# Kernel tuning notes

Hardware: AMD Instinct MI355X
Metric: run time of the kernel (lower is better)

## Reference

```python
import jax, jax.numpy as jnp
import numpy as np

B, T = 1024, 320
EEG_CH, GEO_CH, F1, HID, OUT = 64, 18, 8, 32, 4
THETA0, BETA, TAU_A = 0.5, 1.8, 0.36
EPS = 1e-5


def _bn(x, s, b, m, v):
    # eval-mode BatchNorm with running stats (flax default eps 1e-5)
    return (x - m) * jax.lax.rsqrt(v + EPS) * s + b


def _dwconv(x, w, b, groups):
    # depthwise temporal conv, x: (B, T, C), w: (K, 1, C*F1), SAME padding
    y = jax.lax.conv_general_dilated(x, w, (1,), 'SAME', dimension_numbers=('NWC', 'WIO', 'NWC'), feature_group_count=groups)
    return y + b


def _spike(x):
    return jnp.where(x >= 0.0, 1.0, 0.0)


def _forward(x_eeg, x_geo, eeg_conv_w, eeg_conv_b, eeg_bn1_s, eeg_bn1_b, eeg_bn1_m, eeg_bn1_v, eeg_dense_w, eeg_dense_b, eeg_bn2_s, eeg_bn2_b, eeg_bn2_m, eeg_bn2_v, geo_conv_w, geo_conv_b, geo_bn1_s, geo_bn1_b, geo_bn1_m, geo_bn1_v, geo_dense_w, geo_dense_b, geo_bn2_s, geo_bn2_b, geo_bn2_m, geo_bn2_v, gamma, fc1_w, fc1_b, fc2_w, fc2_b):
    Bc = x_eeg.shape[0]
    xe = _bn(_dwconv(x_eeg, eeg_conv_w, eeg_conv_b, EEG_CH), eeg_bn1_s, eeg_bn1_b, eeg_bn1_m, eeg_bn1_v)
    xe = _bn(xe @ eeg_dense_w + eeg_dense_b, eeg_bn2_s, eeg_bn2_b, eeg_bn2_m, eeg_bn2_v)
    eeg_enc = jax.nn.relu(xe)                      # (B, T, HID)
    xg = _bn(_dwconv(x_geo, geo_conv_w, geo_conv_b, GEO_CH), geo_bn1_s, geo_bn1_b, geo_bn1_m, geo_bn1_v)
    xg = _bn(xg @ geo_dense_w + geo_dense_b, geo_bn2_s, geo_bn2_b, geo_bn2_m, geo_bn2_v)
    geo_mod = jax.nn.sigmoid(xg)                   # (B, T, HID)

    def step(carry, inp):
        m1, m2, m3, ma, eta, mli, prev = carry
        ce, cg = inp
        m1 = 0.9 * m1 + ce; s1 = _spike(m1 - 0.7); m1 = m1 * (1.0 - s1)
        m2 = 0.8 * m2 + ce; s2 = _spike(m2 - 0.5); m2 = m2 * (1.0 - s2)
        m3 = 0.6 * m3 + ce; s3 = _spike(m3 - 0.3); m3 = m3 * (1.0 - s3)
        hr = (s1 + s2 + s3) / 3.0
        eta = TAU_A * eta + (1.0 - TAU_A) * prev
        theta = THETA0 + BETA * eta - gamma * cg
        ma = 0.8 * ma + hr
        sa = _spike(ma - theta)
        ma = ma * (1.0 - sa)
        mli = 0.9 * mli + sa
        return (m1, m2, m3, ma, eta, mli, sa), mli

    z = jnp.zeros((Bc, HID), x_eeg.dtype)
    _, seq = jax.lax.scan(step, (z, z, z, z, z, z, z), (jnp.swapaxes(eeg_enc, 0, 1), jnp.swapaxes(geo_mod, 0, 1)))
    seq = jnp.transpose(seq, (1, 2, 0))            # (B, HID, T)
    win = seq.reshape(Bc, HID, 10, 32)
    dp = (jnp.mean(win[..., 16:], -1) - jnp.mean(win[..., :16], -1)).reshape(Bc, HID * 10)
    return jax.nn.elu(dp @ fc1_w + fc1_b) @ fc2_w + fc2_b


def setup_inputs() -> dict:
    ks = iter(jax.random.split(jax.random.key(0), 48))
    def rn(shape, s=1.0):
        return jax.random.normal(next(ks), shape, jnp.float32) * s
    ECH, GCH = EEG_CH * F1, GEO_CH * F1
    return {
        'x_eeg': rn((B, T, EEG_CH)),
        'x_geo': rn((B, T, GEO_CH)),
        'eeg_conv_w': rn((32, 1, ECH), 0.05), 'eeg_conv_b': jnp.zeros((ECH,), jnp.float32),
        'eeg_bn1_s': 1.0 + rn((ECH,), 0.1), 'eeg_bn1_b': rn((ECH,), 0.1),
        'eeg_bn1_m': rn((ECH,), 0.1), 'eeg_bn1_v': 1.0 + 0.1 * jax.random.uniform(next(ks), (ECH,), jnp.float32),
        'eeg_dense_w': rn((ECH, HID), 0.05), 'eeg_dense_b': jnp.zeros((HID,), jnp.float32),
        'eeg_bn2_s': 1.0 + rn((HID,), 0.1), 'eeg_bn2_b': rn((HID,), 0.1),
        'eeg_bn2_m': rn((HID,), 0.1), 'eeg_bn2_v': 1.0 + 0.1 * jax.random.uniform(next(ks), (HID,), jnp.float32),
        'geo_conv_w': rn((32, 1, GCH), 0.05), 'geo_conv_b': jnp.zeros((GCH,), jnp.float32),
        'geo_bn1_s': 1.0 + rn((GCH,), 0.1), 'geo_bn1_b': rn((GCH,), 0.1),
        'geo_bn1_m': rn((GCH,), 0.1), 'geo_bn1_v': 1.0 + 0.1 * jax.random.uniform(next(ks), (GCH,), jnp.float32),
        'geo_dense_w': rn((GCH, HID), 0.05), 'geo_dense_b': jnp.zeros((HID,), jnp.float32),
        'geo_bn2_s': 1.0 + rn((HID,), 0.1), 'geo_bn2_b': rn((HID,), 0.1),
        'geo_bn2_m': rn((HID,), 0.1), 'geo_bn2_v': 1.0 + 0.1 * jax.random.uniform(next(ks), (HID,), jnp.float32),
        'gamma': jnp.full((HID,), 0.5, jnp.float32),
        'fc1_w': rn((HID * 10, 128), 0.05), 'fc1_b': jnp.zeros((128,), jnp.float32),
        'fc2_w': rn((128, OUT), 0.05), 'fc2_b': jnp.zeros((OUT,), jnp.float32),
    }


def reference(x_eeg, x_geo, eeg_conv_w, eeg_conv_b, eeg_bn1_s, eeg_bn1_b, eeg_bn1_m, eeg_bn1_v, eeg_dense_w, eeg_dense_b, eeg_bn2_s, eeg_bn2_b, eeg_bn2_m, eeg_bn2_v, geo_conv_w, geo_conv_b, geo_bn1_s, geo_bn1_b, geo_bn1_m, geo_bn1_v, geo_dense_w, geo_dense_b, geo_bn2_s, geo_bn2_b, geo_bn2_m, geo_bn2_v, gamma, fc1_w, fc1_b, fc2_w, fc2_b):
    return _forward(x_eeg, x_geo, eeg_conv_w, eeg_conv_b, eeg_bn1_s, eeg_bn1_b, eeg_bn1_m, eeg_bn1_v, eeg_dense_w, eeg_dense_b, eeg_bn2_s, eeg_bn2_b, eeg_bn2_m, eeg_bn2_v, geo_conv_w, geo_conv_b, geo_bn1_s, geo_bn1_b, geo_bn1_m, geo_bn1_v, geo_dense_w, geo_dense_b, geo_bn2_s, geo_bn2_b, geo_bn2_m, geo_bn2_v, gamma, fc1_w, fc1_b, fc2_w, fc2_b)
```

## Files before the change

### kernel.cpp

```cpp
#include <hip/hip_runtime.h>
#include <hip/hip_bf16.h>
#include <math.h>

#define BSZ   1024
#define TLEN  320
#define EEGC  64
#define GEOC  18
#define ECH   512
#define GCH   144
#define HID   32
#define KW    32
#define TT    32
#define NT    (TLEN/TT)

#define OFF_ENC  0
#define OFF_MOD  (OFF_ENC + BSZ*TLEN*HID)
#define OFF_DP   (OFF_MOD + BSZ*TLEN*HID)
#define OFF_CWE  (OFF_DP + BSZ*HID*10)
#define OFF_CWG  (OFF_CWE + ECH*KW)
#define OFF_DWE  (OFF_CWG + GCH*KW)
#define OFF_DWG  (OFF_DWE + ECH*HID)
#define OFF_BTE  (OFF_DWG + GCH*HID)
#define OFF_BTG  (OFF_BTE + HID)
#define OFF_GAM  (OFF_BTG + HID)

struct P29 { const float* p[29]; };

__global__ __launch_bounds__(256) void prep_kernel(P29 P, float* __restrict__ ws)
{
    const int tid = threadIdx.x;
    float* convW_e = ws + OFF_CWE;
    float* convW_g = ws + OFF_CWG;
    float* dW_e    = ws + OFF_DWE;
    float* dW_g    = ws + OFF_DWG;

    for (int i = tid; i < ECH * KW; i += 256) {
        int c = i >> 5, k = i & 31;
        float A1 = P.p[2][c] * rsqrtf(P.p[5][c] + 1e-5f);
        convW_e[c * KW + k] = P.p[0][(size_t)k * ECH + c] * A1;
    }
    for (int i = tid; i < GCH * KW; i += 256) {
        int c = i >> 5, k = i & 31;
        float A1 = P.p[14][c] * rsqrtf(P.p[17][c] + 1e-5f);
        convW_g[c * KW + k] = P.p[12][(size_t)k * GCH + c] * A1;
    }
    for (int i = tid; i < ECH * HID; i += 256) {
        int h = i & 31;
        float A2 = P.p[8][h] * rsqrtf(P.p[11][h] + 1e-5f);
        dW_e[i] = P.p[6][i] * A2;
    }
    for (int i = tid; i < GCH * HID; i += 256) {
        int h = i & 31;
        float A2 = P.p[20][h] * rsqrtf(P.p[23][h] + 1e-5f);
        dW_g[i] = P.p[18][i] * A2;
    }
    for (int i = tid; i < HID; i += 256) ws[OFF_GAM + i] = P.p[24][i];

    if (tid < HID) {
        int h = tid;
        float A2 = P.p[8][h] * rsqrtf(P.p[11][h] + 1e-5f);
        float s = 0.f;
        for (int c = 0; c < ECH; ++c) {
            float A1 = P.p[2][c] * rsqrtf(P.p[5][c] + 1e-5f);
            float C1 = (P.p[1][c] - P.p[4][c]) * A1 + P.p[3][c];
            s += C1 * P.p[6][(size_t)c * HID + h];
        }
        ws[OFF_BTE + h] = A2 * (s + P.p[7][h] - P.p[10][h]) + P.p[9][h];
    } else if (tid >= 64 && tid < 64 + HID) {
        int h = tid - 64;
        float A2 = P.p[20][h] * rsqrtf(P.p[23][h] + 1e-5f);
        float s = 0.f;
        for (int c = 0; c < GCH; ++c) {
            float A1 = P.p[14][c] * rsqrtf(P.p[17][c] + 1e-5f);
            float C1 = (P.p[13][c] - P.p[16][c]) * A1 + P.p[15][c];
            s += C1 * P.p[18][(size_t)c * HID + h];
        }
        ws[OFF_BTG + h] = A2 * (s + P.p[19][h] - P.p[22][h]) + P.p[21][h];
    }
}

__device__ __forceinline__ void conv_stream(const float4* __restrict__ xp4,
                                            const float* __restrict__ w,
                                            float* __restrict__ acc)
{
    float4 cur = xp4[0];
    #pragma unroll
    for (int j4 = 0; j4 < 12; ++j4) {
        float4 nxt = (j4 < 11) ? xp4[j4 + 1] : cur;
        #pragma unroll
        for (int i2 = 0; i2 < 4; ++i2) {
            const int i = j4 * 4 + i2;
            const float xv = (i2 == 0) ? cur.x : (i2 == 1) ? cur.y
                           : (i2 == 2) ? cur.z : cur.w;
            const int tlo = (i - 31 > 0) ? (i - 31) : 0;
            const int thi = (i < 15) ? i : 15;
            #pragma unroll
            for (int t = tlo; t <= thi; ++t)
                acc[t] = fmaf(xv, w[i - t], acc[t]);
        }
        cur = nxt;
    }
}

__global__ __launch_bounds__(256, 4)
void path_eeg(const float* __restrict__ x, float* __restrict__ ws)
{
    __shared__ __align__(16) float xsT[16 * 68];
    __shared__ __align__(16) float czs[128 * 36];

    const int b   = blockIdx.y;
    const int t0  = blockIdx.x * TT;
    const int tid = threadIdx.x;
    const float* convW = ws + OFF_CWE;
    const float* dW    = ws + OFF_DWE;
    float* enc         = ws + OFF_ENC;
    float* cz          = czs;

    const float* xb = x + (size_t)b * (TLEN * EEGC);

    const int tg = tid & 7, hg = (tid >> 3) & 7, q = tid >> 6;
    const int c_loc = tid & 127, th = tid >> 7;
    float a00=0,a01=0,a02=0,a03=0, a10=0,a11=0,a12=0,a13=0;
    float a20=0,a21=0,a22=0,a23=0, a30=0,a31=0,a32=0,a33=0;

    #pragma unroll 1
    for (int ph = 0; ph < 4; ++ph) {
        if (ph) __syncthreads();
        if (tid < 252) {
            const int sj = tid >> 2, sc4 = tid & 3;
            const int st = t0 - 15 + sj;
            float4 sv = make_float4(0.f, 0.f, 0.f, 0.f);
            if (st >= 0 && st < TLEN)
                sv = *(const float4*)(xb + (size_t)st * EEGC + ph * 16 + sc4 * 4);
            float* p = &xsT[(sc4 * 4) * 68 + sj];
            p[0] = sv.x; p[68] = sv.y; p[136] = sv.z; p[204] = sv.w;
        }
        __syncthreads();
        {
            const int c   = ph * 128 + c_loc;
            const int chl = c_loc >> 3;
            float w[KW];
            const float4* wp4 = (const float4*)(convW + c * KW);
            #pragma unroll
            for (int k4 = 0; k4 < 8; ++k4) {
                float4 v = wp4[k4];
                w[4*k4+0]=v.x; w[4*k4+1]=v.y; w[4*k4+2]=v.z; w[4*k4+3]=v.w;
            }
            float acc[16];
            #pragma unroll
            for (int t = 0; t < 16; ++t) acc[t] = 0.f;
            conv_stream((const float4*)(&xsT[chl * 68 + th * 16]), w, acc);
            float4* czp = (float4*)(cz + c_loc * 36 + th * 16);
            czp[0] = make_float4(acc[0],  acc[1],  acc[2],  acc[3]);
            czp[1] = make_float4(acc[4],  acc[5],  acc[6],  acc[7]);
            czp[2] = make_float4(acc[8],  acc[9],  acc[10], acc[11]);
            czp[3] = make_float4(acc[12], acc[13], acc[14], acc[15]);
        }
        __syncthreads();
        {
            const float* dWh = dW + (size_t)(ph * 128 + q * 32) * HID + hg * 4;
            const float* czb = cz + (q * 32) * 36 + tg * 4;
            float4 wvb[4], cvb[2];
            wvb[0] = *(const float4*)(dWh + 0 * HID);
            wvb[1] = *(const float4*)(dWh + 1 * HID);
            wvb[2] = *(const float4*)(dWh + 2 * HID);
            wvb[3] = *(const float4*)(dWh + 3 * HID);
            cvb[0] = *(const float4*)(czb + 0 * 36);
            cvb[1] = *(const float4*)(czb + 1 * 36);
            #pragma unroll
            for (int ci = 0; ci < 32; ++ci) {
                float4 cv = cvb[ci & 1];
                float4 wv = wvb[ci & 3];
                if (ci + 2 < 32) cvb[ci & 1] = *(const float4*)(czb + (ci + 2) * 36);
                if (ci + 4 < 32) wvb[ci & 3] = *(const float4*)(dWh + (ci + 4) * HID);
                a00 = fmaf(cv.x, wv.x, a00); a01 = fmaf(cv.x, wv.y, a01);
                a02 = fmaf(cv.x, wv.z, a02); a03 = fmaf(cv.x, wv.w, a03);
                a10 = fmaf(cv.y, wv.x, a10); a11 = fmaf(cv.y, wv.y, a11);
                a12 = fmaf(cv.y, wv.z, a12); a13 = fmaf(cv.y, wv.w, a13);
                a20 = fmaf(cv.z, wv.x, a20); a21 = fmaf(cv.z, wv.y, a21);
                a22 = fmaf(cv.z, wv.z, a22); a23 = fmaf(cv.z, wv.w, a23);
                a30 = fmaf(cv.w, wv.x, a30); a31 = fmaf(cv.w, wv.y, a31);
                a32 = fmaf(cv.w, wv.z, a32); a33 = fmaf(cv.w, wv.w, a33);
            }
        }
    }

    __syncthreads();
    float* stash = czs;
    {
        const int s = (tid >> 1) & 3;
        float4* sp = (float4*)(stash + tid * 16);
        sp[s ^ 0] = make_float4(a00,a01,a02,a03);
        sp[s ^ 1] = make_float4(a10,a11,a12,a13);
        sp[s ^ 2] = make_float4(a20,a21,a22,a23);
        sp[s ^ 3] = make_float4(a30,a31,a32,a33);
    }
    __syncthreads();
    {
        const int t = tid >> 3, hq = tid & 7;
        const int pg = (t & 3) ^ (t >> 3);
        float4 v = make_float4(0.f,0.f,0.f,0.f);
        #pragma unroll
        for (int qq = 0; qq < 4; ++qq) {
            const int partner = qq * 64 + hq * 8 + (t >> 2);
            float4 s = *(const float4*)(stash + partner * 16 + pg * 4);
            v.x += s.x; v.y += s.y; v.z += s.z; v.w += s.w;
        }
        float4 bias = *(const float4*)(ws + OFF_BTE + hq * 4);
        v.x = fmaxf(v.x + bias.x, 0.f);
        v.y = fmaxf(v.y + bias.y, 0.f);
        v.z = fmaxf(v.z + bias.z, 0.f);
        v.w = fmaxf(v.w + bias.w, 0.f);
        *(float4*)(enc + ((size_t)(b * TLEN + t0 + t)) * HID + hq * 4) = v;
    }
}

__global__ __launch_bounds__(256, 4) void path_geo(const float* __restrict__ x,
                                                   float* __restrict__ ws)
{
    __shared__ __align__(16) float xs[63 * GEOC];
    __shared__ __align__(16) float cz[GCH * 36];

    const int b   = blockIdx.y;
    const int t0  = blockIdx.x * TT;
    const int tid = threadIdx.x;
    const float* convW = ws + OFF_CWG;
    const float* dW    = ws + OFF_DWG;
    float* mod         = ws + OFF_MOD;

    const float* xb = x + (size_t)b * (TLEN * GEOC);
    for (int i = tid; i < 63 * GEOC; i += 256) {
        int j = i / GEOC, ch = i - j * GEOC;
        int t = t0 - 15 + j;
        xs[i] = (t >= 0 && t < TLEN) ? xb[(size_t)t * GEOC + ch] : 0.f;
    }
    __syncthreads();

    if (tid < GCH) {
        const int c  = tid;
        const int ch = c >> 3;
        float w[KW];
        const float4* wp4 = (const float4*)(convW + c * KW);
        #pragma unroll
        for (int k4 = 0; k4 < 8; ++k4) {
            float4 v = wp4[k4];
            w[4*k4+0]=v.x; w[4*k4+1]=v.y; w[4*k4+2]=v.z; w[4*k4+3]=v.w;
        }
        #pragma unroll 1
        for (int th = 0; th < 2; ++th) {
            float xw[47];
            #pragma unroll
            for (int i = 0; i < 47; ++i) xw[i] = xs[(th*16 + i) * GEOC + ch];
            float acc[16];
            #pragma unroll
            for (int t = 0; t < 16; ++t) acc[t] = 0.f;
            #pragma unroll
            for (int k = 0; k < KW; ++k) {
                #pragma unroll
                for (int t = 0; t < 16; ++t)
                    acc[t] = fmaf(xw[t + k], w[k], acc[t]);
            }
            float4* czp = (float4*)(cz + tid * 36 + th * 16);
            czp[0] = make_float4(acc[0],  acc[1],  acc[2],  acc[3]);
            czp[1] = make_float4(acc[4],  acc[5],  acc[6],  acc[7]);
            czp[2] = make_float4(acc[8],  acc[9],  acc[10], acc[11]);
            czp[3] = make_float4(acc[12], acc[13], acc[14], acc[15]);
        }
    }
    __syncthreads();

    const int tg = tid & 7, hg = (tid >> 3) & 7, q = tid >> 6;
    float a00=0,a01=0,a02=0,a03=0, a10=0,a11=0,a12=0,a13=0;
    float a20=0,a21=0,a22=0,a23=0, a30=0,a31=0,a32=0,a33=0;
    {
        const float* dWh = dW + (size_t)(q * 36) * HID + hg * 4;
        const float* czb = cz + (q * 36) * 36 + tg * 4;
        #pragma unroll 2
        for (int ci = 0; ci < 36; ++ci) {
            float4 cv = *(const float4*)(czb + ci * 36);
            float4 wv = *(const float4*)(dWh + ci * HID);
            a00 = fmaf(cv.x, wv.x, a00); a01 = fmaf(cv.x, wv.y, a01);
            a02 = fmaf(cv.x, wv.z, a02); a03 = fmaf(cv.x, wv.w, a03);
            a10 = fmaf(cv.y, wv.x, a10); a11 = fmaf(cv.y, wv.y, a11);
            a12 = fmaf(cv.y, wv.z, a12); a13 = fmaf(cv.y, wv.w, a13);
            a20 = fmaf(cv.z, wv.x, a20); a21 = fmaf(cv.z, wv.y, a21);
            a22 = fmaf(cv.z, wv.z, a22); a23 = fmaf(cv.z, wv.w, a23);
            a30 = fmaf(cv.w, wv.x, a30); a31 = fmaf(cv.w, wv.y, a31);
            a32 = fmaf(cv.w, wv.z, a32); a33 = fmaf(cv.w, wv.w, a33);
        }
    }
    __syncthreads();
    float* stash = cz;
    {
        float4* sp = (float4*)(stash + tid * 20);
        sp[0] = make_float4(a00,a01,a02,a03);
        sp[1] = make_float4(a10,a11,a12,a13);
        sp[2] = make_float4(a20,a21,a22,a23);
        sp[3] = make_float4(a30,a31,a32,a33);
    }
    __syncthreads();
    {
        const int t = tid >> 3, hq = tid & 7;
        float4 v = make_float4(0.f,0.f,0.f,0.f);
        #pragma unroll
        for (int qq = 0; qq < 4; ++qq) {
            const int partner = qq * 64 + hq * 8 + (t >> 2);
            float4 s = *(const float4*)(stash + partner * 20 + (t & 3) * 4);
            v.x += s.x; v.y += s.y; v.z += s.z; v.w += s.w;
        }
        float4 bias = *(const float4*)(ws + OFF_BTG + hq * 4);
        v.x = 1.f / (1.f + expf(-(v.x + bias.x)));
        v.y = 1.f / (1.f + expf(-(v.y + bias.y)));
        v.z = 1.f / (1.f + expf(-(v.z + bias.z)));
        v.w = 1.f / (1.f + expf(-(v.w + bias.w)));
        *(float4*)(mod + ((size_t)(b * TLEN + t0 + t)) * HID + hq * 4) = v;
    }
}

__global__ __launch_bounds__(128) void scan_kernel(float* __restrict__ ws)
{
    const int idx = blockIdx.x * 128 + threadIdx.x;
    const int b = idx >> 5, h = idx & 31;
    const float g = ws[OFF_GAM + h];
    const float* pe = ws + OFF_ENC + (size_t)b * TLEN * HID + h;
    const float* pg = ws + OFF_MOD + (size_t)b * TLEN * HID + h;
    float m1 = 0.f, m2 = 0.f, m3 = 0.f, ma = 0.f, eta = 0.f, mli = 0.f, prev = 0.f;
    float acc_lo = 0.f, acc_hi = 0.f;
    float* dpp = ws + OFF_DP + b * (HID * 10) + h * 10;
    int w = 0;
    #pragma unroll 8
    for (int t = 0; t < TLEN; ++t) {
        const float ce = pe[t * HID];
        const float cg = pg[t * HID];
        m1 = 0.9f * m1 + ce; float s1 = ((m1 - 0.7f) >= 0.f) ? 1.f : 0.f; m1 = m1 * (1.f - s1);
        m2 = 0.8f * m2 + ce; float s2 = ((m2 - 0.5f) >= 0.f) ? 1.f : 0.f; m2 = m2 * (1.f - s2);
        m3 = 0.6f * m3 + ce; float s3 = ((m3 - 0.3f) >= 0.f) ? 1.f : 0.f; m3 = m3 * (1.f - s3);
        const float hr = (s1 + s2 + s3) / 3.0f;
        eta = 0.36f * eta + 0.64f * prev;
        const float theta = 0.5f + 1.8f * eta - g * cg;
        ma = 0.8f * ma + hr;
        const float sa = ((ma - theta) >= 0.f) ? 1.f : 0.f;
        ma = ma * (1.f - sa);
        mli = 0.9f * mli + sa;
        prev = sa;
        if ((t & 31) < 16) acc_lo += mli; else acc_hi += mli;
        if ((t & 31) == 31) {
            dpp[w] = acc_hi * (1.f / 16.f) - acc_lo * (1.f / 16.f);
            acc_lo = 0.f; acc_hi = 0.f; ++w;
        }
    }
}

__global__ __launch_bounds__(128) void head_kernel(
    const float* __restrict__ ws,
    const float* __restrict__ f1w, const float* __restrict__ f1b,
    const float* __restrict__ f2w, const float* __restrict__ f2b,
    float* __restrict__ out)
{
    __shared__ float act[128];
    const int b = blockIdx.x, j = threadIdx.x;
    const float* dpb = ws + OFF_DP + b * 320;
    float a = f1b[j];
    for (int i = 0; i < 320; ++i)
        a = fmaf(dpb[i], f1w[i * 128 + j], a);
    act[j] = (a > 0.f) ? a : expm1f(a);
    __syncthreads();
    if (j < 4) {
        float o = f2b[j];
        for (int jj = 0; jj < 128; ++jj)
            o = fmaf(act[jj], f2w[jj * 4 + j], o);
        out[b * 4 + j] = o;
    }
}

extern "C" void kernel_launch(void* const* d_in, const int* in_sizes, int n_in,
                              void* d_out, int out_size, void* d_ws, size_t ws_size,
                              hipStream_t stream)
{
    float* ws = (float*)d_ws;

    P29 P;
    for (int k = 0; k < 29; ++k) P.p[k] = (const float*)d_in[k + 2];
    prep_kernel<<<1, 256, 0, stream>>>(P, ws);

    path_eeg<<<dim3(NT, BSZ), 256, 0, stream>>>((const float*)d_in[0], ws);
    path_geo<<<dim3(NT, BSZ), 256, 0, stream>>>((const float*)d_in[1], ws);

    scan_kernel<<<(BSZ * HID) / 128, 128, 0, stream>>>(ws);

    head_kernel<<<BSZ, 128, 0, stream>>>(
        ws, (const float*)d_in[27], (const float*)d_in[28],
        (const float*)d_in[29], (const float*)d_in[30], (float*)d_out);
}
```

Measured before the change: 802.9 us.

## Transpose geo input tile in LDS and split conv across all threads

The geo depthwise conv previously ran on only 144 of 256 threads, each computing two 16-step halves serially from a strided LDS layout. The input tile is now stored channel-major (padded to 68) so a shared conv_stream helper can read contiguous float4 windows. Work is split into (channel, half) units spread over all 256 threads, with 32 threads taking a second unit. This raises parallelism and vectorises LDS reads, at the cost of reloading the weights per unit and some load imbalance.

```diff
diff --git a/kernel.cpp b/kernel.cpp
--- a/kernel.cpp
+++ b/kernel.cpp
@@ -215,10 +215,33 @@
     }
 }
 
+__device__ __forceinline__ void geo_conv_unit(const float* __restrict__ convW,
+                                              const float* __restrict__ xsT,
+                                              float* __restrict__ cz,
+                                              int c, int th)
+{
+    float w[KW];
+    const float4* wp4 = (const float4*)(convW + c * KW);
+    #pragma unroll
+    for (int k4 = 0; k4 < 8; ++k4) {
+        float4 v = wp4[k4];
+        w[4*k4+0]=v.x; w[4*k4+1]=v.y; w[4*k4+2]=v.z; w[4*k4+3]=v.w;
+    }
+    float acc[16];
+    #pragma unroll
+    for (int t = 0; t < 16; ++t) acc[t] = 0.f;
+    conv_stream((const float4*)(xsT + (c >> 3) * 68 + th * 16), w, acc);
+    float4* czp = (float4*)(cz + c * 36 + th * 16);
+    czp[0] = make_float4(acc[0],  acc[1],  acc[2],  acc[3]);
+    czp[1] = make_float4(acc[4],  acc[5],  acc[6],  acc[7]);
+    czp[2] = make_float4(acc[8],  acc[9],  acc[10], acc[11]);
+    czp[3] = make_float4(acc[12], acc[13], acc[14], acc[15]);
+}
+
 __global__ __launch_bounds__(256, 4) void path_geo(const float* __restrict__ x,
                                                    float* __restrict__ ws)
 {
-    __shared__ __align__(16) float xs[63 * GEOC];
+    __shared__ __align__(16) float xsT[GEOC * 68];
     __shared__ __align__(16) float cz[GCH * 36];
 
     const int b   = blockIdx.y;
@@ -232,41 +255,13 @@
     for (int i = tid; i < 63 * GEOC; i += 256) {
         int j = i / GEOC, ch = i - j * GEOC;
         int t = t0 - 15 + j;
-        xs[i] = (t >= 0 && t < TLEN) ? xb[(size_t)t * GEOC + ch] : 0.f;
-    }
-    __syncthreads();
-
-    if (tid < GCH) {
-        const int c  = tid;
-        const int ch = c >> 3;
-        float w[KW];
-        const float4* wp4 = (const float4*)(convW + c * KW);
-        #pragma unroll
-        for (int k4 = 0; k4 < 8; ++k4) {
-            float4 v = wp4[k4];
-            w[4*k4+0]=v.x; w[4*k4+1]=v.y; w[4*k4+2]=v.z; w[4*k4+3]=v.w;
-        }
-        #pragma unroll 1
-        for (int th = 0; th < 2; ++th) {
-            float xw[47];
-            #pragma unroll
-            for (int i = 0; i < 47; ++i) xw[i] = xs[(th*16 + i) * GEOC + ch];
-            float acc[16];
-            #pragma unroll
-            for (int t = 0; t < 16; ++t) acc[t] = 0.f;
-            #pragma unroll
-            for (int k = 0; k < KW; ++k) {
-                #pragma unroll
-                for (int t = 0; t < 16; ++t)
-                    acc[t] = fmaf(xw[t + k], w[k], acc[t]);
-            }
-            float4* czp = (float4*)(cz + tid * 36 + th * 16);
-            czp[0] = make_float4(acc[0],  acc[1],  acc[2],  acc[3]);
-            czp[1] = make_float4(acc[4],  acc[5],  acc[6],  acc[7]);
-            czp[2] = make_float4(acc[8],  acc[9],  acc[10], acc[11]);
-            czp[3] = make_float4(acc[12], acc[13], acc[14], acc[15]);
-        }
-    }
+        xsT[ch * 68 + j] = (t >= 0 && t < TLEN) ? xb[(size_t)t * GEOC + ch] : 0.f;
+    }
+    __syncthreads();
+
+    geo_conv_unit(convW, xsT, cz, tid >> 1, tid & 1);
+    if (tid < 32)
+        geo_conv_unit(convW, xsT, cz, 128 + (tid >> 1), tid & 1);
     __syncthreads();
 
     const int tg = tid & 7, hg = (tid >> 3) & 7, q = tid >> 6;
```

New measurement: 840.6 us. 4.7% more time.
